# Performance work log

Measured on AMD Instinct MI355X. Metric: run time of the kernel, lower is better.

The kernel has to match this reference:

```python
import jax, jax.numpy as jnp
import numpy as np

NUM_EMBEDDINGS = 1024
EMBEDDING_DIM = 64
COMMITMENT_COST = 0.25


def setup_inputs() -> dict:
    key = jax.random.key(0)
    k1, k2 = jax.random.split(key)
    z = jax.random.normal(k1, (16, EMBEDDING_DIM, 64, 64), dtype=jnp.float32)
    # nn.Embedding init: uniform(-1/K, 1/K)
    emb = jax.random.uniform(
        k2, (NUM_EMBEDDINGS, EMBEDDING_DIM), dtype=jnp.float32,
        minval=-1.0 / NUM_EMBEDDINGS, maxval=1.0 / NUM_EMBEDDINGS)
    return {"z": z, "emb": emb}


def reference(z, emb):
    # b c h w -> b h w c
    zc = jnp.transpose(z, (0, 2, 3, 1))
    B, H, W, D = zc.shape
    zf = zc.reshape(-1, D)  # [N, D]
    K = emb.shape[0]

    # L2 distances: ||z||^2 + ||e||^2 - 2 z e^T   -> [N, K]
    distances = (jnp.sum(zf * zf, axis=1, keepdims=True)
                 + jnp.sum(emb * emb, axis=1)
                 - 2.0 * jnp.matmul(zf, emb.T))
    encoding_indices = jnp.argmin(distances, axis=1)  # [N]

    # one_hot @ emb  ==  gather
    quantized = emb[encoding_indices].reshape(zc.shape)  # [B,H,W,D]

    reconstruction_errors = jnp.sum((quantized - zc) ** 2, axis=-1).reshape(-1)
    avg_error = jnp.mean(reconstruction_errors)

    e_latent_loss = jnp.mean((jax.lax.stop_gradient(quantized) - zc) ** 2)
    q_latent_loss = jnp.mean((quantized - jax.lax.stop_gradient(zc)) ** 2)
    loss = q_latent_loss + COMMITMENT_COST * e_latent_loss

    # straight-through estimator
    quantized_st = zc + jax.lax.stop_gradient(quantized - zc)
    out = jnp.transpose(quantized_st, (0, 3, 1, 2))  # b h w c -> b c h w

    # perplexity: avg one-hot usage (histogram instead of dense one-hot)
    N = zf.shape[0]
    counts = jnp.zeros((K,), dtype=jnp.float32).at[encoding_indices].add(1.0)
    avg_probs = counts / N
    perplexity = jnp.exp(-jnp.sum(avg_probs * jnp.log(avg_probs + 1e-10)))

    return out, loss, perplexity, avg_error
```

## Files before the change

kernel.cpp:

```cpp
#include <hip/hip_runtime.h>
#include <stdint.h>

#define HW   4096
#define NEMB 1024

typedef float        f32x4  __attribute__((ext_vector_type(4)));
typedef short        h16x8  __attribute__((ext_vector_type(8)));
typedef unsigned int u32x4  __attribute__((ext_vector_type(4)));

#define CVTPKH(D, LO, HI) asm("v_cvt_pkrtz_f16_f32 %0, %1, %2" : "=v"(D) : "v"(LO), "v"(HI))

__device__ __forceinline__ void gload_lds16(const float* g, float* l) {
    __builtin_amdgcn_global_load_lds(
        (const __attribute__((address_space(1))) void*)(uintptr_t)g,
        (__attribute__((address_space(3))) void*)(uintptr_t)l, 16, 0, 0);
}

__global__ __launch_bounds__(128) void vq_init(const float* __restrict__ emb,
                                               unsigned int* __restrict__ counts,
                                               float* __restrict__ errsum,
                                               float* __restrict__ ens1,
                                               unsigned int* __restrict__ embh) {
    const int k = blockIdx.x * 128 + threadIdx.x;
    counts[k] = 0u;
    if (k == 0) *errsum = 0.0f;
    const float* e = emb + k * 64;
    unsigned int* dst = embh + k * 32;
    float a[8] = {0,0,0,0,0,0,0,0};
    #pragma unroll
    for (int c = 0; c < 8; ++c) {
        f32x4 v0 = *(const f32x4*)(e + c * 8);
        f32x4 v1 = *(const f32x4*)(e + c * 8 + 4);
        a[0] += v0.x * v0.x; a[1] += v0.y * v0.y;
        a[2] += v0.z * v0.z; a[3] += v0.w * v0.w;
        a[4] += v1.x * v1.x; a[5] += v1.y * v1.y;
        a[6] += v1.z * v1.z; a[7] += v1.w * v1.w;
        u32x4 w;
        CVTPKH(w.x, v0.x, v0.y); CVTPKH(w.y, v0.z, v0.w);
        CVTPKH(w.z, v1.x, v1.y); CVTPKH(w.w, v1.z, v1.w);
        *(u32x4*)&dst[c * 4] = w;
    }
    ens1[k] = 1.0f + (((a[0]+a[1]) + (a[2]+a[3])) + ((a[4]+a[5]) + (a[6]+a[7])));
}

__global__ __launch_bounds__(512, 4)
void vq_main(const float* __restrict__ z, const float* __restrict__ emb,
             const float* __restrict__ ens1, const unsigned int* __restrict__ embh,
             float* __restrict__ out, unsigned int* __restrict__ counts,
             float* __restrict__ errsum)
{
    __shared__ __attribute__((aligned(16))) float z_lds[64 * 128];
    __shared__ __attribute__((aligned(16))) unsigned int zh[128 * 32];
    __shared__ __attribute__((aligned(16))) float ens_lds[NEMB];
    __shared__ unsigned int kd[8][128];
    __shared__ int   idx_sh[128];
    __shared__ float errp[512];

    const int t   = threadIdx.x;
    const int n0  = blockIdx.x * 128;
    const int bb  = n0 >> 12;
    const int hw0 = n0 & 4095;
    const float* zb = z + bb * (64 * HW) + hw0;

    #pragma unroll
    for (int it = 0; it < 4; ++it) {
        const int p = it * 512 + t;
        gload_lds16(zb + (p >> 5) * HW + (p & 31) * 4, z_lds + p * 4);
    }
    if (t < 256) gload_lds16(ens1 + t * 4, ens_lds + t * 4);
    __syncthreads();

    {
        const int x = t & 127;
        #pragma unroll
        for (int ss = 0; ss < 2; ++ss) {
            const int s = (x + (t >> 7) * 2 + ss) & 7;
            const int c = s ^ (x & 7);
            u32x4 w;
            CVTPKH(w.x, z_lds[(8*c + 0) * 128 + x], z_lds[(8*c + 1) * 128 + x]);
            CVTPKH(w.y, z_lds[(8*c + 2) * 128 + x], z_lds[(8*c + 3) * 128 + x]);
            CVTPKH(w.z, z_lds[(8*c + 4) * 128 + x], z_lds[(8*c + 5) * 128 + x]);
            CVTPKH(w.w, z_lds[(8*c + 6) * 128 + x], z_lds[(8*c + 7) * 128 + x]);
            *(u32x4*)&zh[x * 32 + s * 4] = w;
        }
    }

    const int l   = t & 63;
    const int wv  = t >> 6;
    const int col = l & 15;
    const int bg  = l >> 4;

    u32x4 bw0[8], bw1[8];
    {
        const unsigned int* ebase = embh + (wv * 128 + col) * 32 + bg * 4;
        #pragma unroll
        for (int g = 0; g < 8; ++g) {
            bw0[g] = *(const u32x4*)(ebase + g * 16 * 32);
            bw1[g] = *(const u32x4*)(ebase + g * 16 * 32 + 16);
        }
    }
    float en[8];
    #pragma unroll
    for (int g = 0; g < 8; ++g) en[g] = ens_lds[wv * 128 + g * 16 + col];

    __syncthreads();

    const unsigned int lkc = (unsigned int)col;
    #pragma unroll 1
    for (int st = 0; st < 8; ++st) {
        const int xs = st * 16 + col;
        const int sA = bg ^ (col & 7);
        u32x4 wa = *(const u32x4*)&zh[xs * 32 + sA * 4];
        u32x4 wb = *(const u32x4*)&zh[xs * 32 + (sA ^ 4) * 4];
        h16x8 a0 = __builtin_bit_cast(h16x8, wa);
        h16x8 a1 = __builtin_bit_cast(h16x8, wb);

        unsigned int k0 = ~0u, k1 = ~0u, k2 = ~0u, k3 = ~0u;
        #pragma unroll
        for (int g = 0; g < 8; ++g) {
            f32x4 cc = {0.0f, 0.0f, 0.0f, 0.0f};
            cc = __builtin_amdgcn_mfma_f32_16x16x32_f16(a0, __builtin_bit_cast(h16x8, bw0[g]), cc, 0, 0, 0);
            cc = __builtin_amdgcn_mfma_f32_16x16x32_f16(a1, __builtin_bit_cast(h16x8, bw1[g]), cc, 0, 0, 0);
            const unsigned int lk = (unsigned int)(g << 4) | lkc;
            float s0 = fmaf(-2.0f, cc[0], en[g]);
            float s1 = fmaf(-2.0f, cc[1], en[g]);
            float s2 = fmaf(-2.0f, cc[2], en[g]);
            float s3 = fmaf(-2.0f, cc[3], en[g]);
            unsigned int q0 = (__builtin_bit_cast(unsigned int, s0) & ~127u) | lk;
            unsigned int q1 = (__builtin_bit_cast(unsigned int, s1) & ~127u) | lk;
            unsigned int q2 = (__builtin_bit_cast(unsigned int, s2) & ~127u) | lk;
            unsigned int q3 = (__builtin_bit_cast(unsigned int, s3) & ~127u) | lk;
            k0 = k0 < q0 ? k0 : q0;  k1 = k1 < q1 ? k1 : q1;
            k2 = k2 < q2 ? k2 : q2;  k3 = k3 < q3 ? k3 : q3;
        }
        #pragma unroll
        for (int mk = 1; mk <= 8; mk <<= 1) {
            unsigned int o0 = (unsigned int)__shfl_xor((int)k0, mk, 64);
            unsigned int o1 = (unsigned int)__shfl_xor((int)k1, mk, 64);
            unsigned int o2 = (unsigned int)__shfl_xor((int)k2, mk, 64);
            unsigned int o3 = (unsigned int)__shfl_xor((int)k3, mk, 64);
            k0 = k0 < o0 ? k0 : o0;  k1 = k1 < o1 ? k1 : o1;
            k2 = k2 < o2 ? k2 : o2;  k3 = k3 < o3 ? k3 : o3;
        }
        if (col == 0) {
            u32x4 kv = {k0, k1, k2, k3};
            *(u32x4*)&kd[wv][st * 16 + bg * 4] = kv;
        }
    }
    __syncthreads();

    if (t < 128) {
        unsigned int kw = kd[0][t];
        unsigned int bv = kw & ~127u;
        int bk = (int)(kw & 127u);
        #pragma unroll
        for (int w = 1; w < 8; ++w) {
            kw = kd[w][t];
            unsigned int vw = kw & ~127u;
            int kk = w * 128 + (int)(kw & 127u);
            if (vw < bv || (vw == bv && kk < bk)) { bv = vw; bk = kk; }
        }
        idx_sh[t] = bk;
        atomicAdd(&counts[bk], 1u);
    }
    __syncthreads();

    {
        const int x  = t & 127;
        const int cg = t >> 7;
        const int idx = idx_sh[x];
        const float* er = emb + idx * 64;
        float* ob = out + bb * (64 * HW) + hw0 + x;
        float part = 0.0f;
        #pragma unroll
        for (int cq = 0; cq < 4; ++cq) {
            const int c = cg * 16 + cq * 4;
            f32x4 e4 = *(const f32x4*)&er[c];
            float z0 = z_lds[(c+0) * 128 + x];
            float z1 = z_lds[(c+1) * 128 + x];
            float z2 = z_lds[(c+2) * 128 + x];
            float z3 = z_lds[(c+3) * 128 + x];
            ob[(c+0) * HW] = z0 + (e4.x - z0);
            ob[(c+1) * HW] = z1 + (e4.y - z1);
            ob[(c+2) * HW] = z2 + (e4.z - z2);
            ob[(c+3) * HW] = z3 + (e4.w - z3);
            float d0 = z0 - e4.x, d1 = z1 - e4.y, d2 = z2 - e4.z, d3 = z3 - e4.w;
            part = fmaf(d0, d0, part); part = fmaf(d1, d1, part);
            part = fmaf(d2, d2, part); part = fmaf(d3, d3, part);
        }
        errp[t] = part;
    }
    __syncthreads();
    if (t < 128) {
        float s = (errp[t] + errp[t + 128]) + (errp[t + 256] + errp[t + 384]);
        #pragma unroll
        for (int off = 32; off >= 1; off >>= 1) s += __shfl_down(s, off, 64);
        if ((t & 63) == 0) atomicAdd(errsum, s);
    }
}

__global__ __launch_bounds__(256) void vq_fin(const unsigned int* __restrict__ counts,
                                              const float* __restrict__ errsum,
                                              float* __restrict__ scal)
{
    __shared__ float part[4];
    const int t = threadIdx.x;
    float s = 0.0f;
    for (int k = t; k < NEMB; k += 256) {
        float p = (float)counts[k] * (1.0f / 65536.0f);
        s += p * logf(p + 1e-10f);
    }
    #pragma unroll
    for (int off = 32; off >= 1; off >>= 1) s += __shfl_down(s, off, 64);
    if ((t & 63) == 0) part[t >> 6] = s;
    __syncthreads();
    if (t == 0) {
        float tot = (part[0] + part[1]) + (part[2] + part[3]);
        float es  = *errsum;
        scal[0] = 1.25f * (es * (1.0f / 4194304.0f));
        scal[1] = expf(-tot);
        scal[2] = es * (1.0f / 65536.0f);
    }
}

extern "C" void kernel_launch(void* const* d_in, const int* in_sizes, int n_in,
                              void* d_out, int out_size, void* d_ws, size_t ws_size,
                              hipStream_t stream) {
    const float* z   = (const float*)d_in[0];
    const float* emb = (const float*)d_in[1];
    float* out = (float*)d_out;
    unsigned int* counts = (unsigned int*)d_ws;
    float* errsum = (float*)((char*)d_ws + 4096);
    float* ens1   = (float*)((char*)d_ws + 8192);
    unsigned int* embh = (unsigned int*)((char*)d_ws + 16384);

    vq_init<<<8, 128, 0, stream>>>(emb, counts, errsum, ens1, embh);
    vq_main<<<512, 512, 0, stream>>>(z, emb, ens1, embh, out, counts, errsum);
    vq_fin<<<1, 256, 0, stream>>>(counts, errsum, out + 4194304);
}
```

Measured before the change: 44.13 us.

## Split VQ main kernel into codebook-quartered screen and separate output kernel

The fused kernel is replaced by two kernels. A screen kernel launches 4x more blocks, each handling a quarter of the codebook for a 128-row tile, and merges per-row argmin keys globally with atomicMin on packed value|index keys, now using 10 index bits. A separate output kernel gathers the chosen embeddings, writes the output, and accumulates error and counts. The aim is more parallelism and occupancy in the distance search. The cost is a second read of z, global atomics on the keys, an extra launch, and coarser distance quantisation from masking 10 low bits.

```diff
diff --git a/kernel.cpp b/kernel.cpp
--- a/kernel.cpp
+++ b/kernel.cpp
@@ -9,127 +9,120 @@
 typedef unsigned int u32x4  __attribute__((ext_vector_type(4)));
 
 #define CVTPKH(D, LO, HI) asm("v_cvt_pkrtz_f16_f32 %0, %1, %2" : "=v"(D) : "v"(LO), "v"(HI))
-
-__device__ __forceinline__ void gload_lds16(const float* g, float* l) {
-    __builtin_amdgcn_global_load_lds(
-        (const __attribute__((address_space(1))) void*)(uintptr_t)g,
-        (__attribute__((address_space(3))) void*)(uintptr_t)l, 16, 0, 0);
-}
 
 __global__ __launch_bounds__(128) void vq_init(const float* __restrict__ emb,
                                                unsigned int* __restrict__ counts,
                                                float* __restrict__ errsum,
                                                float* __restrict__ ens1,
-                                               unsigned int* __restrict__ embh) {
-    const int k = blockIdx.x * 128 + threadIdx.x;
-    counts[k] = 0u;
-    if (k == 0) *errsum = 0.0f;
-    const float* e = emb + k * 64;
-    unsigned int* dst = embh + k * 32;
-    float a[8] = {0,0,0,0,0,0,0,0};
-    #pragma unroll
-    for (int c = 0; c < 8; ++c) {
+                                               unsigned int* __restrict__ embh,
+                                               unsigned int* __restrict__ keys) {
+    const int gid  = blockIdx.x * 128 + threadIdx.x;
+    const int k    = gid >> 1;
+    const int half = gid & 1;
+    if (half == 0) counts[k] = 0u;
+    if (gid == 0) *errsum = 0.0f;
+    {
+        u32x4 ff = {~0u, ~0u, ~0u, ~0u};
+        #pragma unroll
+        for (int i = 0; i < 8; ++i)
+            *(u32x4*)&keys[gid * 32 + i * 4] = ff;
+    }
+    const float* e = emb + k * 64 + half * 32;
+    unsigned int* dst = embh + k * 32 + half * 16;
+    float nrm = 0.0f;
+    #pragma unroll
+    for (int c = 0; c < 4; ++c) {
         f32x4 v0 = *(const f32x4*)(e + c * 8);
         f32x4 v1 = *(const f32x4*)(e + c * 8 + 4);
-        a[0] += v0.x * v0.x; a[1] += v0.y * v0.y;
-        a[2] += v0.z * v0.z; a[3] += v0.w * v0.w;
-        a[4] += v1.x * v1.x; a[5] += v1.y * v1.y;
-        a[6] += v1.z * v1.z; a[7] += v1.w * v1.w;
+        nrm += v0.x*v0.x + v0.y*v0.y + v0.z*v0.z + v0.w*v0.w
+             + v1.x*v1.x + v1.y*v1.y + v1.z*v1.z + v1.w*v1.w;
         u32x4 w;
         CVTPKH(w.x, v0.x, v0.y); CVTPKH(w.y, v0.z, v0.w);
         CVTPKH(w.z, v1.x, v1.y); CVTPKH(w.w, v1.z, v1.w);
         *(u32x4*)&dst[c * 4] = w;
     }
-    ens1[k] = 1.0f + (((a[0]+a[1]) + (a[2]+a[3])) + ((a[4]+a[5]) + (a[6]+a[7])));
-}
-
-__global__ __launch_bounds__(512, 4)
-void vq_main(const float* __restrict__ z, const float* __restrict__ emb,
-             const float* __restrict__ ens1, const unsigned int* __restrict__ embh,
-             float* __restrict__ out, unsigned int* __restrict__ counts,
-             float* __restrict__ errsum)
+    float o = __shfl_xor(nrm, 1, 64);
+    if (half == 0) ens1[k] = 1.0f + (nrm + o);
+}
+
+__global__ __launch_bounds__(256, 4)
+void vq_screen(const float* __restrict__ z, const float* __restrict__ ens1,
+               const unsigned int* __restrict__ embh,
+               unsigned int* __restrict__ keys)
 {
-    __shared__ __attribute__((aligned(16))) float z_lds[64 * 128];
-    __shared__ __attribute__((aligned(16))) unsigned int zh[128 * 32];
-    __shared__ __attribute__((aligned(16))) float ens_lds[NEMB];
-    __shared__ unsigned int kd[8][128];
-    __shared__ int   idx_sh[128];
-    __shared__ float errp[512];
-
-    const int t   = threadIdx.x;
-    const int n0  = blockIdx.x * 128;
-    const int bb  = n0 >> 12;
-    const int hw0 = n0 & 4095;
+    __shared__ __attribute__((aligned(16))) unsigned int zh[128 * 36];
+    __shared__ __attribute__((aligned(16))) unsigned int kd[4][128];
+
+    const int t    = threadIdx.x;
+    const int bid  = blockIdx.x;
+    const int tile = bid >> 2;
+    const int q    = bid & 3;
+    const int n0   = tile * 128;
+    const int bb   = n0 >> 12;
+    const int hw0  = n0 & 4095;
     const float* zb = z + bb * (64 * HW) + hw0;
-
-    #pragma unroll
-    for (int it = 0; it < 4; ++it) {
-        const int p = it * 512 + t;
-        gload_lds16(zb + (p >> 5) * HW + (p & 31) * 4, z_lds + p * 4);
-    }
-    if (t < 256) gload_lds16(ens1 + t * 4, ens_lds + t * 4);
-    __syncthreads();
-
-    {
-        const int x = t & 127;
-        #pragma unroll
-        for (int ss = 0; ss < 2; ++ss) {
-            const int s = (x + (t >> 7) * 2 + ss) & 7;
-            const int c = s ^ (x & 7);
-            u32x4 w;
-            CVTPKH(w.x, z_lds[(8*c + 0) * 128 + x], z_lds[(8*c + 1) * 128 + x]);
-            CVTPKH(w.y, z_lds[(8*c + 2) * 128 + x], z_lds[(8*c + 3) * 128 + x]);
-            CVTPKH(w.z, z_lds[(8*c + 4) * 128 + x], z_lds[(8*c + 5) * 128 + x]);
-            CVTPKH(w.w, z_lds[(8*c + 6) * 128 + x], z_lds[(8*c + 7) * 128 + x]);
-            *(u32x4*)&zh[x * 32 + s * 4] = w;
-        }
-    }
 
     const int l   = t & 63;
     const int wv  = t >> 6;
     const int col = l & 15;
     const int bg  = l >> 4;
 
-    u32x4 bw0[8], bw1[8];
-    {
-        const unsigned int* ebase = embh + (wv * 128 + col) * 32 + bg * 4;
-        #pragma unroll
-        for (int g = 0; g < 8; ++g) {
-            bw0[g] = *(const u32x4*)(ebase + g * 16 * 32);
-            bw1[g] = *(const u32x4*)(ebase + g * 16 * 32 + 16);
-        }
-    }
-    float en[8];
-    #pragma unroll
-    for (int g = 0; g < 8; ++g) en[g] = ens_lds[wv * 128 + g * 16 + col];
-
-    __syncthreads();
-
-    const unsigned int lkc = (unsigned int)col;
+    u32x4 b0[4], b1[4];
+    float en[4];
+    {
+        const int row0 = q * 256 + wv * 64 + col;
+        #pragma unroll
+        for (int cg = 0; cg < 4; ++cg) {
+            const unsigned int* eb = embh + (row0 + cg * 16) * 32 + bg * 4;
+            b0[cg] = *(const u32x4*)eb;
+            b1[cg] = *(const u32x4*)(eb + 16);
+            en[cg] = ens1[row0 + cg * 16];
+        }
+    }
+    #pragma unroll
+    for (int cg = 0; cg < 4; ++cg)
+        asm volatile("" : "+v"(b0[cg]), "+v"(b1[cg]), "+v"(en[cg]));
+
+    {
+        const int x  = t & 127;
+        const int hf = t >> 7;
+        #pragma unroll
+        for (int ci = 0; ci < 4; ++ci) {
+            const int c = hf * 4 + ci;
+            u32x4 w;
+            CVTPKH(w.x, zb[(8*c + 0) * HW + x], zb[(8*c + 1) * HW + x]);
+            CVTPKH(w.y, zb[(8*c + 2) * HW + x], zb[(8*c + 3) * HW + x]);
+            CVTPKH(w.z, zb[(8*c + 4) * HW + x], zb[(8*c + 5) * HW + x]);
+            CVTPKH(w.w, zb[(8*c + 6) * HW + x], zb[(8*c + 7) * HW + x]);
+            *(u32x4*)&zh[x * 36 + ((c ^ (x & 7)) << 2)] = w;
+        }
+    }
+    __syncthreads();
+
     #pragma unroll 1
     for (int st = 0; st < 8; ++st) {
         const int xs = st * 16 + col;
-        const int sA = bg ^ (col & 7);
-        u32x4 wa = *(const u32x4*)&zh[xs * 32 + sA * 4];
-        u32x4 wb = *(const u32x4*)&zh[xs * 32 + (sA ^ 4) * 4];
+        const int sA = bg ^ (xs & 7);
+        u32x4 wa = *(const u32x4*)&zh[xs * 36 + sA * 4];
+        u32x4 wb = *(const u32x4*)&zh[xs * 36 + (sA ^ 4) * 4];
         h16x8 a0 = __builtin_bit_cast(h16x8, wa);
         h16x8 a1 = __builtin_bit_cast(h16x8, wb);
 
         unsigned int k0 = ~0u, k1 = ~0u, k2 = ~0u, k3 = ~0u;
         #pragma unroll
-        for (int g = 0; g < 8; ++g) {
+        for (int cg = 0; cg < 4; ++cg) {
             f32x4 cc = {0.0f, 0.0f, 0.0f, 0.0f};
-            cc = __builtin_amdgcn_mfma_f32_16x16x32_f16(a0, __builtin_bit_cast(h16x8, bw0[g]), cc, 0, 0, 0);
-            cc = __builtin_amdgcn_mfma_f32_16x16x32_f16(a1, __builtin_bit_cast(h16x8, bw1[g]), cc, 0, 0, 0);
-            const unsigned int lk = (unsigned int)(g << 4) | lkc;
-            float s0 = fmaf(-2.0f, cc[0], en[g]);
-            float s1 = fmaf(-2.0f, cc[1], en[g]);
-            float s2 = fmaf(-2.0f, cc[2], en[g]);
-            float s3 = fmaf(-2.0f, cc[3], en[g]);
-            unsigned int q0 = (__builtin_bit_cast(unsigned int, s0) & ~127u) | lk;
-            unsigned int q1 = (__builtin_bit_cast(unsigned int, s1) & ~127u) | lk;
-            unsigned int q2 = (__builtin_bit_cast(unsigned int, s2) & ~127u) | lk;
-            unsigned int q3 = (__builtin_bit_cast(unsigned int, s3) & ~127u) | lk;
+            cc = __builtin_amdgcn_mfma_f32_16x16x32_f16(a0, __builtin_bit_cast(h16x8, b0[cg]), cc, 0, 0, 0);
+            cc = __builtin_amdgcn_mfma_f32_16x16x32_f16(a1, __builtin_bit_cast(h16x8, b1[cg]), cc, 0, 0, 0);
+            const unsigned int kk = (unsigned int)(q * 256 + wv * 64 + cg * 16 + col);
+            float s0 = fmaf(-2.0f, cc[0], en[cg]);
+            float s1 = fmaf(-2.0f, cc[1], en[cg]);
+            float s2 = fmaf(-2.0f, cc[2], en[cg]);
+            float s3 = fmaf(-2.0f, cc[3], en[cg]);
+            unsigned int q0 = (__builtin_bit_cast(unsigned int, s0) & ~1023u) | kk;
+            unsigned int q1 = (__builtin_bit_cast(unsigned int, s1) & ~1023u) | kk;
+            unsigned int q2 = (__builtin_bit_cast(unsigned int, s2) & ~1023u) | kk;
+            unsigned int q3 = (__builtin_bit_cast(unsigned int, s3) & ~1023u) | kk;
             k0 = k0 < q0 ? k0 : q0;  k1 = k1 < q1 ? k1 : q1;
             k2 = k2 < q2 ? k2 : q2;  k3 = k3 < q3 ? k3 : q3;
         }
@@ -150,53 +143,57 @@
     __syncthreads();
 
     if (t < 128) {
-        unsigned int kw = kd[0][t];
-        unsigned int bv = kw & ~127u;
-        int bk = (int)(kw & 127u);
-        #pragma unroll
-        for (int w = 1; w < 8; ++w) {
-            kw = kd[w][t];
-            unsigned int vw = kw & ~127u;
-            int kk = w * 128 + (int)(kw & 127u);
-            if (vw < bv || (vw == bv && kk < bk)) { bv = vw; bk = kk; }
-        }
-        idx_sh[t] = bk;
-        atomicAdd(&counts[bk], 1u);
-    }
-    __syncthreads();
-
-    {
-        const int x  = t & 127;
-        const int cg = t >> 7;
-        const int idx = idx_sh[x];
-        const float* er = emb + idx * 64;
-        float* ob = out + bb * (64 * HW) + hw0 + x;
-        float part = 0.0f;
-        #pragma unroll
-        for (int cq = 0; cq < 4; ++cq) {
-            const int c = cg * 16 + cq * 4;
-            f32x4 e4 = *(const f32x4*)&er[c];
-            float z0 = z_lds[(c+0) * 128 + x];
-            float z1 = z_lds[(c+1) * 128 + x];
-            float z2 = z_lds[(c+2) * 128 + x];
-            float z3 = z_lds[(c+3) * 128 + x];
-            ob[(c+0) * HW] = z0 + (e4.x - z0);
-            ob[(c+1) * HW] = z1 + (e4.y - z1);
-            ob[(c+2) * HW] = z2 + (e4.z - z2);
-            ob[(c+3) * HW] = z3 + (e4.w - z3);
-            float d0 = z0 - e4.x, d1 = z1 - e4.y, d2 = z2 - e4.z, d3 = z3 - e4.w;
-            part = fmaf(d0, d0, part); part = fmaf(d1, d1, part);
-            part = fmaf(d2, d2, part); part = fmaf(d3, d3, part);
-        }
-        errp[t] = part;
-    }
-    __syncthreads();
-    if (t < 128) {
-        float s = (errp[t] + errp[t + 128]) + (errp[t + 256] + errp[t + 384]);
+        unsigned int ka = kd[0][t] < kd[1][t] ? kd[0][t] : kd[1][t];
+        unsigned int kb = kd[2][t] < kd[3][t] ? kd[2][t] : kd[3][t];
+        atomicMin(&keys[n0 + t], ka < kb ? ka : kb);
+    }
+}
+
+__global__ __launch_bounds__(256)
+void vq_out(const float* __restrict__ z, const float* __restrict__ emb,
+            const unsigned int* __restrict__ keys,
+            float* __restrict__ out, unsigned int* __restrict__ counts,
+            float* __restrict__ errsum)
+{
+    __shared__ float errw[4];
+    const int t   = threadIdx.x;
+    const int n0  = blockIdx.x * 128;
+    const int bb  = n0 >> 12;
+    const int hw0 = n0 & 4095;
+    const int x   = t & 127;
+    const int cg  = t >> 7;
+
+    const int idx = (int)(keys[n0 + x] & 1023u);
+    if (t < 128) atomicAdd(&counts[idx], 1u);
+
+    const float* er = emb + idx * 64;
+    const float* zp = z + bb * (64 * HW) + hw0 + x;
+    float* ob = out + bb * (64 * HW) + hw0 + x;
+    float part = 0.0f;
+    #pragma unroll
+    for (int cq = 0; cq < 8; ++cq) {
+        const int c = cg * 32 + cq * 4;
+        f32x4 e4 = *(const f32x4*)&er[c];
+        float z0 = zp[(c+0) * HW];
+        float z1 = zp[(c+1) * HW];
+        float z2 = zp[(c+2) * HW];
+        float z3 = zp[(c+3) * HW];
+        ob[(c+0) * HW] = z0 + (e4.x - z0);
+        ob[(c+1) * HW] = z1 + (e4.y - z1);
+        ob[(c+2) * HW] = z2 + (e4.z - z2);
+        ob[(c+3) * HW] = z3 + (e4.w - z3);
+        float d0 = z0 - e4.x, d1 = z1 - e4.y, d2 = z2 - e4.z, d3 = z3 - e4.w;
+        part = fmaf(d0, d0, part); part = fmaf(d1, d1, part);
+        part = fmaf(d2, d2, part); part = fmaf(d3, d3, part);
+    }
+    {
+        float s = part;
         #pragma unroll
         for (int off = 32; off >= 1; off >>= 1) s += __shfl_down(s, off, 64);
-        if ((t & 63) == 0) atomicAdd(errsum, s);
-    }
+        if ((t & 63) == 0) errw[t >> 6] = s;
+    }
+    __syncthreads();
+    if (t == 0) atomicAdd(errsum, (errw[0] + errw[1]) + (errw[2] + errw[3]));
 }
 
 __global__ __launch_bounds__(256) void vq_fin(const unsigned int* __restrict__ counts,
@@ -233,8 +230,10 @@
     float* errsum = (float*)((char*)d_ws + 4096);
     float* ens1   = (float*)((char*)d_ws + 8192);
     unsigned int* embh = (unsigned int*)((char*)d_ws + 16384);
-
-    vq_init<<<8, 128, 0, stream>>>(emb, counts, errsum, ens1, embh);
-    vq_main<<<512, 512, 0, stream>>>(z, emb, ens1, embh, out, counts, errsum);
+    unsigned int* keys = (unsigned int*)((char*)d_ws + 147456);
+
+    vq_init<<<16, 128, 0, stream>>>(emb, counts, errsum, ens1, embh, keys);
+    vq_screen<<<2048, 256, 0, stream>>>(z, ens1, embh, keys);
+    vq_out<<<512, 256, 0, stream>>>(z, emb, keys, out, counts, errsum);
     vq_fin<<<1, 256, 0, stream>>>(counts, errsum, out + 4194304);
 }
```

Measured after the change: 58.41 us. +32.4%, slower.
